# Optimization experiments

Hardware: AMD Instinct MI355X
Metric: run time of the kernel (lower is better)

Reference implementation:

```python
import jax, jax.numpy as jnp
import numpy as np

DECAY = 0.1
EPS = 1e-5


def setup_inputs() -> dict:
    key = jax.random.key(0)
    k1, k2, k3 = jax.random.split(key, 3)
    H, N, D, K = 1, 32768, 256, 4096
    x = jax.random.normal(k1, (H, N, D), dtype=jnp.float32)
    embed = jax.random.normal(k2, (H, K, D), dtype=jnp.float32) * 0.01
    cluster_size = jnp.ones((H, K), dtype=jnp.float32)
    embed_avg = jax.random.normal(k3, (H, K, D), dtype=jnp.float32) * 0.01
    return {"x": x, "embed": embed, "cluster_size": cluster_size, "embed_avg": embed_avg}


def reference(x, embed, cluster_size, embed_avg):
    # x: [H, N, D] flattened latents; embed: [H, K, D] codebook
    H, N, D = x.shape
    K = embed.shape[1]

    x_sq = jnp.sum(x * x, axis=-1, keepdims=True)          # [H, N, 1]
    e_sq = jnp.sum(embed * embed, axis=-1)[:, None, :]     # [H, 1, K]
    dist = x_sq - 2.0 * jnp.einsum('hnd,hkd->hnk', x, embed) + e_sq

    embed_ind = jnp.argmin(dist, axis=-1)                  # [H, N] int

    # gather nearest code vectors: [H, N, D]
    quantize = jax.vmap(lambda e, i: e[i])(embed, embed_ind)

    # EMA statistics (no_grad in torch): bincount + scatter-add of latents
    bins = jax.vmap(lambda i: jax.ops.segment_sum(jnp.ones((N,), x.dtype), i, num_segments=K))(embed_ind)                      # [H, K]
    embed_sum = jax.vmap(lambda xh, ih: jax.ops.segment_sum(xh, ih, num_segments=K))(x, embed_ind)                             # [H, K, D]

    new_cluster_size = cluster_size * DECAY + bins * (1.0 - DECAY)
    new_embed_avg = embed_avg * DECAY + embed_sum * (1.0 - DECAY)

    # laplace-smoothed normalization of codebook
    n = jnp.sum(new_cluster_size, axis=-1, keepdims=True)
    smoothed = (new_cluster_size + EPS) / (n + K * EPS) * n
    embed_normalized = new_embed_avg / smoothed[..., None]  # [H, K, D]

    # commitment loss (quantize detached) and straight-through output
    commit_loss = jnp.mean((jax.lax.stop_gradient(quantize) - x) ** 2)
    out = x + jax.lax.stop_gradient(quantize - x)

    return out, commit_loss, embed_ind, new_cluster_size, embed_normalized
```

## Files before the change

### kernel.cpp

```cpp
#include <hip/hip_runtime.h>
#include <hip/hip_bf16.h>
#include <cstdint>
#include <cstddef>

#define NROWS 32768
#define DDIM 256
#define KCODES 4096

typedef __attribute__((ext_vector_type(8))) short s16x8;
typedef __attribute__((ext_vector_type(4))) float f32x4;
typedef unsigned long long u64;
typedef unsigned int u32;

#define WS_LOSS 0
#define WS_CNT 1
#define WS_EMAX 2
#define WS_DISTRUST 3
#define WS_NSC 4
#define WS_HIST 8
#define WS_OFFS 4104
#define WS_CURSOR 8200
#define WS_LPART 12296
#define WS_RLIST 16392
#define WS_ESUM 49160
#define WS_XSQ 1097736
#define WS_ESQ 1130504
#define WS_IDX 1134600
#define WS_KEY 1167368
#define WS_TKEY 1232904
#define WS_TM2 1757192
#define WS_LIST 2019336
#define WS_EH 2052104
#define WS_EL 2576392
#define WS_TOTAL 3100680
#define WS_ZERO_FLOATS 12296

__device__ __forceinline__ float hsum16_np(const float a[16]) {
    float t3[8];
#pragma unroll
    for (int m = 0; m < 8; ++m) t3[m] = __fadd_rn(a[m + 8], a[m]);
    float t6[4];
#pragma unroll
    for (int m = 0; m < 4; ++m) t6[m] = __fadd_rn(t3[m + 4], t3[m]);
    return __fadd_rn(__fadd_rn(t6[0], t6[2]), __fadd_rn(t6[1], t6[3]));
}

__device__ __forceinline__ float np_sum_sq_128(const float* a) {
    float t[16];
#pragma unroll
    for (int l = 0; l < 16; ++l) {
        float m0 = __fmul_rn(a[l], a[l]);
        float m1 = __fmul_rn(a[16 + l], a[16 + l]);
        float m2 = __fmul_rn(a[32 + l], a[32 + l]);
        float m3 = __fmul_rn(a[48 + l], a[48 + l]);
        float m4 = __fmul_rn(a[64 + l], a[64 + l]);
        float m5 = __fmul_rn(a[80 + l], a[80 + l]);
        float m6 = __fmul_rn(a[96 + l], a[96 + l]);
        float m7 = __fmul_rn(a[112 + l], a[112 + l]);
        float s01 = __fadd_rn(m0, m1);
        float s23 = __fadd_rn(m2, m3);
        float s45 = __fadd_rn(m4, m5);
        float s67 = __fadd_rn(m6, m7);
        t[l] = __fadd_rn(__fadd_rn(s01, s23), __fadd_rn(s45, s67));
    }
    return hsum16_np(t);
}

__global__ void k_rownorm(const float* __restrict__ src, float* __restrict__ dst, int rows) {
    int r = blockIdx.x * blockDim.x + threadIdx.x;
    if (r < rows) {
        const float* p = src + ((size_t)r << 8);
        dst[r] = __fadd_rn(np_sum_sq_128(p), np_sum_sq_128(p + 128));
    }
}

__global__ void k_emax(const float* __restrict__ esq, float* __restrict__ emax) {
    __shared__ float s[1024];
    int t = threadIdx.x;
    float m = 0.0f;
    for (int i = t; i < KCODES; i += 1024) m = fmaxf(m, esq[i]);
    s[t] = m;
    __syncthreads();
    for (int w = 512; w > 0; w >>= 1) {
        if (t < w) s[t] = fmaxf(s[t], s[t + w]);
        __syncthreads();
    }
    if (t == 0) emax[0] = s[0];
}

__device__ __forceinline__ ushort bf16_rn(float x) {
    u32 u = __float_as_uint(x);
    u32 r = (u + 0x7fffu + ((u >> 16) & 1u)) >> 16;
    return (ushort)r;
}
__device__ __forceinline__ float bf16_f(ushort h) { return __uint_as_float(((u32)h) << 16); }

__global__ void k_pack(const float* __restrict__ src, ushort* __restrict__ hi,
                       ushort* __restrict__ lo) {
    int i = (blockIdx.x * 256 + threadIdx.x) * 8;
    float4 v0 = *reinterpret_cast<const float4*>(src + i);
    float4 v1 = *reinterpret_cast<const float4*>(src + i + 4);
    float f[8] = {v0.x, v0.y, v0.z, v0.w, v1.x, v1.y, v1.z, v1.w};
    ushort h[8], l[8];
#pragma unroll
    for (int j = 0; j < 8; ++j) {
        h[j] = bf16_rn(f[j]);
        l[j] = bf16_rn(__fsub_rn(f[j], bf16_f(h[j])));
    }
    *reinterpret_cast<s16x8*>(hi + i) = *reinterpret_cast<s16x8*>(h);
    *reinterpret_cast<s16x8*>(lo + i) = *reinterpret_cast<s16x8*>(l);
}

__device__ __forceinline__ float keyval_(u64 k) {
    u32 u = (u32)(k >> 32);
    u = (u & 0x80000000u) ? (u ^ 0x80000000u) : ~u;
    return __uint_as_float(u);
}
__device__ __forceinline__ u64 packkey(float d, u32 j) {
    u32 u = __float_as_uint(d);
    u ^= (u32)((int)u >> 31) | 0x80000000u;
    return ((u64)u << 32) | j;
}
#define KEY_INIT 0xFF8000007FFFFFFFull

__device__ __forceinline__ void dma16(const void* g, void* l) {
    __builtin_amdgcn_global_load_lds(
        (const __attribute__((address_space(1))) void*)g,
        (__attribute__((address_space(3))) void*)l, 16, 0, 0);
}

__global__ __attribute__((amdgpu_flat_work_group_size(512, 512), amdgpu_waves_per_eu(4, 4)))
void k_mfma(const ushort* __restrict__ xh_g, const ushort* __restrict__ xl_g,
            const ushort* __restrict__ eh_g, const ushort* __restrict__ el_g,
            const float* __restrict__ xsq, const float* __restrict__ esq,
            u64* __restrict__ tkey, float* __restrict__ tm2) {
    __shared__ __align__(16) ushort xh_s[16384];
    __shared__ __align__(16) ushort xl_s[16384];
    __shared__ __align__(16) ushort eh_s[4096];
    __shared__ __align__(16) ushort el_s[4096];

    const int tid = threadIdx.x;
    const int w = tid >> 6, l = tid & 63, lr = l & 15, lg = l >> 4;
    const int n0 = blockIdx.x * 256, jb = blockIdx.y, j0 = jb * 512;
    const int key = (lr & 7) << 4;

    float xq[8];
#pragma unroll
    for (int i = 0; i < 8; ++i)
        xq[i] = xsq[n0 + w * 32 + (i >> 2) * 16 + lg * 4 + (i & 3)];

    u64 K1[8];
    float M2[8];
#pragma unroll
    for (int i = 0; i < 8; ++i) { K1[i] = KEY_INIT; M2[i] = __uint_as_float(0x7F800000u); }

    for (int js = 0; js < 8; ++js) {
        const int jbase = j0 + js * 64;
        f32x4 acc[2][4];
#pragma unroll
        for (int a = 0; a < 2; ++a)
#pragma unroll
            for (int b = 0; b < 4; ++b) acc[a][b] = (f32x4){0.f, 0.f, 0.f, 0.f};

        for (int c = 0; c < 4; ++c) {
            __syncthreads();
#pragma unroll
            for (int p = 0; p < 4; ++p) {
                int m = tid + p * 512, r = m >> 3, cb = (m & 7) << 4;
                int so = (n0 + r) * 256 + c * 64 + ((cb ^ ((r & 7) << 4)) >> 1);
                dma16(xh_g + so, (char*)xh_s + m * 16);
                dma16(xl_g + so, (char*)xl_s + m * 16);
            }
            {
                int m = tid, r = m >> 3, cb = (m & 7) << 4;
                int so = (jbase + r) * 256 + c * 64 + ((cb ^ ((r & 7) << 4)) >> 1);
                dma16(eh_g + so, (char*)eh_s + m * 16);
                dma16(el_g + so, (char*)el_s + m * 16);
            }
            __syncthreads();
#pragma unroll
            for (int ks = 0; ks < 2; ++ks) {
                const int off = (ks * 64 + lg * 16) ^ key;
                s16x8 axh[2], axl[2];
#pragma unroll
                for (int ns = 0; ns < 2; ++ns) {
                    const int row = w * 32 + ns * 16 + lr;
                    axh[ns] = *(const s16x8*)((const char*)(xh_s + row * 64) + off);
                    axl[ns] = *(const s16x8*)((const char*)(xl_s + row * 64) + off);
                }
#pragma unroll
                for (int jp = 0; jp < 2; ++jp) {
                    s16x8 beh[2], bel[2];
#pragma unroll
                    for (int q = 0; q < 2; ++q) {
                        const int row = (jp * 2 + q) * 16 + lr;
                        beh[q] = *(const s16x8*)((const char*)(eh_s + row * 64) + off);
                        bel[q] = *(const s16x8*)((const char*)(el_s + row * 64) + off);
                    }
#pragma unroll
                    for (int q = 0; q < 2; ++q) {
                        const int jsub = jp * 2 + q;
#pragma unroll
                        for (int ns = 0; ns < 2; ++ns) {
                            acc[ns][jsub] = __builtin_amdgcn_mfma_f32_16x16x32_bf16(
                                axh[ns], beh[q], acc[ns][jsub], 0, 0, 0);
                            acc[ns][jsub] = __builtin_amdgcn_mfma_f32_16x16x32_bf16(
                                axh[ns], bel[q], acc[ns][jsub], 0, 0, 0);
                            acc[ns][jsub] = __builtin_amdgcn_mfma_f32_16x16x32_bf16(
                                axl[ns], beh[q], acc[ns][jsub], 0, 0, 0);
                        }
                    }
                }
            }
        }
#pragma unroll
        for (int jsub = 0; jsub < 4; ++jsub) {
            const int j = jbase + jsub * 16 + lr;
            const float eq = esq[j];
#pragma unroll
            for (int ns = 0; ns < 2; ++ns)
#pragma unroll
                for (int r = 0; r < 4; ++r) {
                    const float s = acc[ns][jsub][r];
                    const float d = __fadd_rn(__fsub_rn(xq[ns * 4 + r], __fmul_rn(2.0f, s)), eq);
                    const u64 kk = packkey(d, (u32)j);
                    const int i8 = ns * 4 + r;
                    if (kk < K1[i8]) { M2[i8] = keyval_(K1[i8]); K1[i8] = kk; }
                    else if (d < M2[i8]) M2[i8] = d;
                }
        }
    }
#pragma unroll
    for (int i8 = 0; i8 < 8; ++i8) {
        u64 k1 = K1[i8];
        float m2 = M2[i8];
#pragma unroll
        for (int mk = 1; mk < 16; mk <<= 1) {
            u32 klo = __shfl_xor((u32)k1, mk);
            u32 khi = __shfl_xor((u32)(k1 >> 32), mk);
            float om2 = __shfl_xor(m2, mk);
            u64 ok = ((u64)khi << 32) | klo;
            if (ok < k1) { m2 = fminf(om2, keyval_(k1)); k1 = ok; }
            else m2 = fminf(m2, keyval_(ok));
        }
        if (lr == 0) {
            const int n = n0 + w * 32 + (i8 >> 2) * 16 + lg * 4 + (i8 & 3);
            tkey[(size_t)jb * NROWS + n] = k1;
            tm2[(size_t)jb * NROWS + n] = m2;
        }
    }
}

__global__ void k_merge(const u64* __restrict__ tkey, const float* __restrict__ tm2,
                        const float* __restrict__ xsq, const float* __restrict__ emaxp,
                        u64* __restrict__ key64, u32* __restrict__ list, u32* __restrict__ cnt) {
    const int n = blockIdx.x * 256 + threadIdx.x;
    u64 k1 = tkey[n];
    float m2 = tm2[n];
#pragma unroll
    for (int jb = 1; jb < 8; ++jb) {
        u64 ok = tkey[(size_t)jb * NROWS + n];
        float om2 = tm2[(size_t)jb * NROWS + n];
        if (ok < k1) { m2 = fminf(om2, keyval_(k1)); k1 = ok; }
        else m2 = fminf(m2, keyval_(ok));
    }
    const float B = sqrtf(xsq[n] * emaxp[0]);
    const float Ed = 2.4e-4f * B + 1.5e-4f;
    if (m2 - keyval_(k1) <= 2.0f * Ed) {
        key64[n] = ~0ull;
        list[atomicAdd(cnt, 1u)] = (u32)n;
    } else {
        key64[n] = k1;
    }
}

__global__ void k_verify(const float* __restrict__ x, const float* __restrict__ e,
                         const float* __restrict__ xsq, const float* __restrict__ esq,
                         const float* __restrict__ emaxp, u64* __restrict__ key64,
                         u32* __restrict__ list, u32* __restrict__ cnt,
                         u32* __restrict__ distrust) {
    const int li = threadIdx.x & 15;
    const int n = blockIdx.x * 16 + (threadIdx.x >> 4);
    const u64 k = key64[n];
    const bool active = (k != ~0ull);
    const int idx = active ? (int)(k & 0xFFFu) : 0;
    const float* xr = x + ((size_t)n << 8);
    const float* er = e + ((size_t)idx << 8);
    float a = 0.0f;
#pragma unroll
    for (int g = 0; g < 4; ++g)
#pragma unroll
        for (int bb = 3; bb >= 0; --bb) {
            const int d = (g * 4 + bb) * 16 + li;
            a = __builtin_fmaf(xr[d], er[d], a);
        }
    const float s1 = __fadd_rn(__shfl_xor(a, 8), a);
    const float s2 = __fadd_rn(__shfl_xor(s1, 4), s1);
    const float u = __fadd_rn(s2, __shfl_xor(s2, 2));
    const float dot = __fadd_rn(u, __shfl_xor(u, 1));
    if (li == 0 && active) {
        const float d = __fadd_rn(__fsub_rn(xsq[n], __fmul_rn(2.0f, dot)), esq[idx]);
        const float dref = keyval_(k);
        const float B = sqrtf(xsq[n] * emaxp[0]);
        const float Ed = 2.4e-4f * B + 1.5e-4f;
        const float diff = fabsf(d - dref);
        if (diff > Ed) {
            key64[n] = ~0ull;
            list[atomicAdd(cnt, 1u)] = (u32)n;
            if (diff > 0.05f) atomicOr(distrust, 1u);
        }
    }
}

__global__ void k_distrust(const u32* __restrict__ distrust, u64* __restrict__ key64,
                           u32* __restrict__ list, u32* __restrict__ cnt) {
    if (*distrust == 0u) return;
    const int n = blockIdx.x * 256 + threadIdx.x;
    key64[n] = ~0ull;
    list[n] = (u32)n;
    if (n == 0) *cnt = (u32)NROWS;
}

__global__ __attribute__((amdgpu_flat_work_group_size(512, 512), amdgpu_waves_per_eu(4)))
void k_exact(const float* __restrict__ x, const float* __restrict__ embed,
             const float* __restrict__ xsq, const float* __restrict__ esq,
             const u32* __restrict__ list, const u32* __restrict__ cntp,
             u64* __restrict__ key64) {
    const u32 cnt = *cntp;
    const int grp = blockIdx.x >> 3, seg = blockIdx.x & 7;
    const u32 base = (u32)grp * 32u;
    if (base >= cnt) return;

    __shared__ float xs[32][260];
    __shared__ float es[64][68];
    u64* red = (u64*)&es[0][0];

    const int tid = threadIdx.x;
    const int lane = tid & 63;
    const int w = tid >> 6;
    const int g = w >> 2;
    const int tc = lane & 15;
    const int tr = ((w & 3) << 2) + (lane >> 4);
    const int cbase = (g << 5) + tc;

#pragma unroll
    for (int p = 0; p < 4; ++p) {
        int v = tid + p * 512;
        int r = v >> 6;
        int c4 = (v & 63) << 2;
        u32 row = list[(base + (u32)r < cnt) ? base + r : base];
        const float4 f = *reinterpret_cast<const float4*>(x + ((size_t)row << 8) + c4);
        *reinterpret_cast<float4*>(&xs[r][c4]) = f;
    }

    const u32 row0 = list[(base + (u32)tr < cnt) ? base + tr : base];
    const u32 row1 = list[(base + (u32)tr + 16u < cnt) ? base + tr + 16 : base];
    const float xq0 = xsq[row0];
    const float xq1 = xsq[row1];

    u64 best0 = ~0ull, best1 = ~0ull;

    for (int ktl = 0; ktl < 8; ++ktl) {
        const int k0 = seg * 512 + ktl * 64;
        float acc[2][2][16];
#pragma unroll
        for (int i = 0; i < 2; ++i)
#pragma unroll
            for (int j = 0; j < 2; ++j)
#pragma unroll
                for (int q = 0; q < 16; ++q) acc[i][j][q] = 0.0f;

        for (int c = 0; c < 4; ++c) {
            __syncthreads();
#pragma unroll
            for (int p = 0; p < 2; ++p) {
                int v = tid + p * 512;
                int r = v >> 4;
                int c4 = (v & 15) << 2;
                const float4 f = *reinterpret_cast<const float4*>(
                    embed + ((size_t)(k0 + r) << 8) + (c << 6) + c4);
                *reinterpret_cast<float4*>(&es[r][c4]) = f;
            }
            __syncthreads();
#pragma unroll
            for (int jj = 3; jj >= 0; --jj) {
#pragma unroll
                for (int q = 0; q < 4; ++q) {
                    const int dl = ((c * 4 + jj) << 4) + (q << 2);
                    const int el = (jj << 4) + (q << 2);
                    const float4 a0 = *reinterpret_cast<const float4*>(&xs[tr][dl]);
                    const float4 a1 = *reinterpret_cast<const float4*>(&xs[tr + 16][dl]);
                    const int lb = q << 2;
#pragma unroll
                    for (int j2 = 0; j2 < 2; ++j2) {
                        const float4 b = *reinterpret_cast<const float4*>(&es[cbase + 16 * j2][el]);
                        acc[0][j2][lb + 0] = __builtin_fmaf(a0.x, b.x, acc[0][j2][lb + 0]);
                        acc[0][j2][lb + 1] = __builtin_fmaf(a0.y, b.y, acc[0][j2][lb + 1]);
                        acc[0][j2][lb + 2] = __builtin_fmaf(a0.z, b.z, acc[0][j2][lb + 2]);
                        acc[0][j2][lb + 3] = __builtin_fmaf(a0.w, b.w, acc[0][j2][lb + 3]);
                        acc[1][j2][lb + 0] = __builtin_fmaf(a1.x, b.x, acc[1][j2][lb + 0]);
                        acc[1][j2][lb + 1] = __builtin_fmaf(a1.y, b.y, acc[1][j2][lb + 1]);
                        acc[1][j2][lb + 2] = __builtin_fmaf(a1.z, b.z, acc[1][j2][lb + 2]);
                        acc[1][j2][lb + 3] = __builtin_fmaf(a1.w, b.w, acc[1][j2][lb + 3]);
                    }
                }
            }
        }
#pragma unroll
        for (int j2 = 0; j2 < 2; ++j2) {
            const int kk = k0 + cbase + 16 * j2;
            const float eq = esq[kk];
            {
                const float dist = __fadd_rn(__fsub_rn(xq0, __fmul_rn(2.0f, hsum16_np(acc[0][j2]))), eq);
                const u64 kkey = packkey(dist, (u32)kk);
                best0 = kkey < best0 ? kkey : best0;
            }
            {
                const float dist = __fadd_rn(__fsub_rn(xq1, __fmul_rn(2.0f, hsum16_np(acc[1][j2]))), eq);
                const u64 kkey = packkey(dist, (u32)kk);
                best1 = kkey < best1 ? kkey : best1;
            }
        }
    }

    __syncthreads();
    red[tr * 32 + (g << 4) + tc] = best0;
    red[(tr + 16) * 32 + (g << 4) + tc] = best1;
    __syncthreads();
    if (tid < 32) {
        u64 m = red[tid * 32];
#pragma unroll
        for (int t = 1; t < 32; ++t) {
            u64 v = red[tid * 32 + t];
            m = v < m ? v : m;
        }
        if (base + (u32)tid < cnt) atomicMin(&key64[list[base + tid]], m);
    }
}

__global__ void k_finhist(const u64* __restrict__ key64, int* __restrict__ idx,
                          u32* __restrict__ hist, float* __restrict__ ind_out) {
    const int n = blockIdx.x * 256 + threadIdx.x;
    const int k = (int)(key64[n] & 0xFFFull);
    idx[n] = k;
    atomicAdd(&hist[k], 1u);
    ind_out[n] = (float)k;
}

__global__ __attribute__((amdgpu_flat_work_group_size(512, 512), amdgpu_waves_per_eu(4)))
void k_argmin_full(const float* __restrict__ x, const float* __restrict__ embed,
                   const float* __restrict__ xsq, const float* __restrict__ esq,
                   int* __restrict__ out_idx) {
    __shared__ float xs[32][260];
    __shared__ float es[64][68];
    u64* red = (u64*)&es[0][0];
    const int tid = threadIdx.x;
    const int lane = tid & 63;
    const int w = tid >> 6;
    const int g = w >> 2;
    const int tc = lane & 15;
    const int tr = ((w & 3) << 2) + (lane >> 4);
    const int cbase = (g << 5) + tc;
    const int n0 = blockIdx.x * 32;
#pragma unroll
    for (int p = 0; p < 4; ++p) {
        int v = tid + p * 512;
        int r = v >> 6;
        int c4 = (v & 63) << 2;
        const float4 f = *reinterpret_cast<const float4*>(x + ((size_t)(n0 + r) << 8) + c4);
        *reinterpret_cast<float4*>(&xs[r][c4]) = f;
    }
    const float xq0 = xsq[n0 + tr];
    const float xq1 = xsq[n0 + tr + 16];
    u64 best0 = ~0ull, best1 = ~0ull;
    for (int kt = 0; kt < KCODES / 64; ++kt) {
        const int k0 = kt * 64;
        float acc[2][2][16];
#pragma unroll
        for (int i = 0; i < 2; ++i)
#pragma unroll
            for (int j = 0; j < 2; ++j)
#pragma unroll
                for (int q = 0; q < 16; ++q) acc[i][j][q] = 0.0f;
        for (int c = 0; c < 4; ++c) {
            __syncthreads();
#pragma unroll
            for (int p = 0; p < 2; ++p) {
                int v = tid + p * 512;
                int r = v >> 4;
                int c4 = (v & 15) << 2;
                const float4 f = *reinterpret_cast<const float4*>(
                    embed + ((size_t)(k0 + r) << 8) + (c << 6) + c4);
                *reinterpret_cast<float4*>(&es[r][c4]) = f;
            }
            __syncthreads();
#pragma unroll
            for (int jj = 3; jj >= 0; --jj) {
#pragma unroll
                for (int q = 0; q < 4; ++q) {
                    const int dl = ((c * 4 + jj) << 4) + (q << 2);
                    const int el = (jj << 4) + (q << 2);
                    const float4 a0 = *reinterpret_cast<const float4*>(&xs[tr][dl]);
                    const float4 a1 = *reinterpret_cast<const float4*>(&xs[tr + 16][dl]);
                    const int lb = q << 2;
#pragma unroll
                    for (int j2 = 0; j2 < 2; ++j2) {
                        const float4 b = *reinterpret_cast<const float4*>(&es[cbase + 16 * j2][el]);
                        acc[0][j2][lb + 0] = __builtin_fmaf(a0.x, b.x, acc[0][j2][lb + 0]);
                        acc[0][j2][lb + 1] = __builtin_fmaf(a0.y, b.y, acc[0][j2][lb + 1]);
                        acc[0][j2][lb + 2] = __builtin_fmaf(a0.z, b.z, acc[0][j2][lb + 2]);
                        acc[0][j2][lb + 3] = __builtin_fmaf(a0.w, b.w, acc[0][j2][lb + 3]);
                        acc[1][j2][lb + 0] = __builtin_fmaf(a1.x, b.x, acc[1][j2][lb + 0]);
                        acc[1][j2][lb + 1] = __builtin_fmaf(a1.y, b.y, acc[1][j2][lb + 1]);
                        acc[1][j2][lb + 2] = __builtin_fmaf(a1.z, b.z, acc[1][j2][lb + 2]);
                        acc[1][j2][lb + 3] = __builtin_fmaf(a1.w, b.w, acc[1][j2][lb + 3]);
                    }
                }
            }
        }
#pragma unroll
        for (int j2 = 0; j2 < 2; ++j2) {
            const int kk = k0 + cbase + 16 * j2;
            const float eq = esq[kk];
            {
                const float dist = __fadd_rn(__fsub_rn(xq0, __fmul_rn(2.0f, hsum16_np(acc[0][j2]))), eq);
                const u64 kkey = packkey(dist, (u32)kk);
                best0 = kkey < best0 ? kkey : best0;
            }
            {
                const float dist = __fadd_rn(__fsub_rn(xq1, __fmul_rn(2.0f, hsum16_np(acc[1][j2]))), eq);
                const u64 kkey = packkey(dist, (u32)kk);
                best1 = kkey < best1 ? kkey : best1;
            }
        }
    }
    __syncthreads();
    red[tr * 32 + (g << 4) + tc] = best0;
    red[(tr + 16) * 32 + (g << 4) + tc] = best1;
    __syncthreads();
    if (tid < 32) {
        u64 m = red[tid * 32];
#pragma unroll
        for (int t = 1; t < 32; ++t) {
            u64 v = red[tid * 32 + t];
            m = v < m ? v : m;
        }
        out_idx[n0 + tid] = (int)(m & 0xFFFFFFFFu);
    }
}

__global__ void k_scan(const u32* __restrict__ hist, u32* __restrict__ offs) {
    __shared__ u32 ts[1024];
    const int t = threadIdx.x;
    const u32 h0 = hist[t * 4], h1 = hist[t * 4 + 1], h2 = hist[t * 4 + 2], h3 = hist[t * 4 + 3];
    const u32 tot = h0 + h1 + h2 + h3;
    ts[t] = tot;
    __syncthreads();
    for (int o = 1; o < 1024; o <<= 1) {
        const u32 add = (t >= o) ? ts[t - o] : 0u;
        __syncthreads();
        ts[t] += add;
        __syncthreads();
    }
    const u32 excl = ts[t] - tot;
    offs[t * 4] = excl;
    offs[t * 4 + 1] = excl + h0;
    offs[t * 4 + 2] = excl + h0 + h1;
    offs[t * 4 + 3] = excl + h0 + h1 + h2;
}

__global__ void k_place(const int* __restrict__ idx, u32* __restrict__ cursor,
                        const u32* __restrict__ offs, u32* __restrict__ rlist) {
    const int n = blockIdx.x * 256 + threadIdx.x;
    const int k = idx[n];
    const u32 p = atomicAdd(&cursor[k], 1u);
    rlist[offs[k] + p] = (u32)n;
}

__global__ void k_esum(const float* __restrict__ x, const u32* __restrict__ rlist,
                       const u32* __restrict__ offs, const u32* __restrict__ hist,
                       float* __restrict__ esum) {
    const int k = blockIdx.x;
    const int d = threadIdx.x;
    const u32 o = offs[k], c = hist[k];
    float s = 0.0f;
    for (u32 i = 0; i < c; ++i) s += x[((size_t)rlist[o + i] << 8) + d];
    esum[((size_t)k << 8) + d] = s;
}

__global__ void k_outloss(const float* __restrict__ x, const float* __restrict__ e,
                          const int* __restrict__ idx, float* __restrict__ out,
                          float* __restrict__ lpart) {
    const int d = threadIdx.x;
    float ls = 0.0f;
#pragma unroll
    for (int r = 0; r < 8; ++r) {
        const int n = blockIdx.x * 8 + r;
        const int k = idx[n];
        const size_t xi = ((size_t)n << 8) + d;
        const float xv = x[xi];
        const float qv = e[((size_t)k << 8) + d];
        const float diff = __fsub_rn(qv, xv);
        out[xi] = __fadd_rn(xv, diff);
        ls = __builtin_fmaf(diff, diff, ls);
    }
    __shared__ float sred[256];
    sred[d] = ls;
    __syncthreads();
    for (int s = 128; s > 0; s >>= 1) {
        if (d < s) sred[d] += sred[d + s];
        __syncthreads();
    }
    if (d == 0) lpart[blockIdx.x] = sred[0];
}

__global__ void k_cluster(const float* __restrict__ cs, const u32* __restrict__ hist,
                          float* __restrict__ ncs_out, float* __restrict__ n_out) {
    __shared__ float sred[1024];
    const int t = threadIdx.x;
    float s = 0.0f;
    for (int k = t; k < KCODES; k += 1024) {
        const float ncs = __fadd_rn(__fmul_rn(cs[k], 0.1f), __fmul_rn((float)hist[k], 0.9f));
        ncs_out[k] = ncs;
        s += ncs;
    }
    sred[t] = s;
    __syncthreads();
    for (int w = 512; w > 0; w >>= 1) {
        if (t < w) sred[t] += sred[t + w];
        __syncthreads();
    }
    if (t == 0) n_out[0] = sred[0];
}

__global__ void k_norm(const float* __restrict__ ea, const float* __restrict__ esum,
                       const float* __restrict__ ncs, const float* __restrict__ nptr,
                       float* __restrict__ en_out) {
    const int i = blockIdx.x * 256 + threadIdx.x;
    const int k = i >> 8;
    const float n = nptr[0];
    const float ncsk = ncs[k];
    const float smoothed = (ncsk + 1e-5f) / (n + 4096.0f * 1e-5f) * n;
    const float nea = __fadd_rn(__fmul_rn(ea[i], 0.1f), __fmul_rn(esum[i], 0.9f));
    en_out[i] = nea / smoothed;
}

__global__ void k_loss(const float* __restrict__ lpart, float* __restrict__ dst) {
    __shared__ float s[256];
    const int t = threadIdx.x;
    float a = 0.0f;
    for (int i = t; i < 4096; i += 256) a += lpart[i];
    s[t] = a;
    __syncthreads();
    for (int w = 128; w > 0; w >>= 1) {
        if (t < w) s[t] += s[t + w];
        __syncthreads();
    }
    if (t == 0) dst[0] = s[0] * (1.0f / 8388608.0f);
}

extern "C" void kernel_launch(void* const* d_in, const int* in_sizes, int n_in, void* d_out,
                              int out_size, void* d_ws, size_t ws_size, hipStream_t stream) {
    (void)in_sizes; (void)n_in; (void)out_size;
    const float* x = (const float*)d_in[0];
    const float* emb = (const float*)d_in[1];
    const float* cs = (const float*)d_in[2];
    const float* ea = (const float*)d_in[3];
    float* ws = (float*)d_ws;
    float* out = (float*)d_out;

    u32* w_cnt = (u32*)(ws + WS_CNT);
    float* w_emax = ws + WS_EMAX;
    u32* w_dis = (u32*)(ws + WS_DISTRUST);
    float* w_n = ws + WS_NSC;
    u32* w_hist = (u32*)(ws + WS_HIST);
    u32* w_offs = (u32*)(ws + WS_OFFS);
    u32* w_cursor = (u32*)(ws + WS_CURSOR);
    float* w_lpart = ws + WS_LPART;
    u32* w_rlist = (u32*)(ws + WS_RLIST);
    float* w_esum = ws + WS_ESUM;
    float* w_xsq = ws + WS_XSQ;
    float* w_esq = ws + WS_ESQ;
    int* w_idx = (int*)(ws + WS_IDX);
    u64* w_key = (u64*)(ws + WS_KEY);
    u64* w_tkey = (u64*)(ws + WS_TKEY);
    float* w_tm2 = ws + WS_TM2;
    u32* w_list = (u32*)(ws + WS_LIST);
    ushort* eh_g = (ushort*)(ws + WS_EH);
    ushort* el_g = (ushort*)(ws + WS_EL);

    float* o_out = out;
    float* o_loss = out + 8388608;
    float* o_ind = out + 8388609;
    float* o_ncs = out + 8421377;
    float* o_en = out + 8425473;

    ushort* xh_g = (ushort*)o_out;
    ushort* xl_g = (ushort*)o_out + 8388608;

    hipMemsetAsync(d_ws, 0, (size_t)WS_ZERO_FLOATS * sizeof(float), stream);

    k_rownorm<<<NROWS / 256, 256, 0, stream>>>(x, w_xsq, NROWS);
    k_rownorm<<<KCODES / 256, 256, 0, stream>>>(emb, w_esq, KCODES);

    if (ws_size >= (size_t)WS_TOTAL * sizeof(float)) {
        k_emax<<<1, 1024, 0, stream>>>(w_esq, w_emax);
        k_pack<<<4096, 256, 0, stream>>>(x, xh_g, xl_g);
        k_pack<<<512, 256, 0, stream>>>(emb, eh_g, el_g);
        k_mfma<<<dim3(128, 8), 512, 0, stream>>>(xh_g, xl_g, eh_g, el_g, w_xsq, w_esq,
                                                 w_tkey, w_tm2);
        k_merge<<<128, 256, 0, stream>>>(w_tkey, w_tm2, w_xsq, w_emax, w_key, w_list, w_cnt);
        k_verify<<<2048, 256, 0, stream>>>(x, emb, w_xsq, w_esq, w_emax, w_key, w_list,
                                           w_cnt, w_dis);
        k_distrust<<<128, 256, 0, stream>>>(w_dis, w_key, w_list, w_cnt);
        k_exact<<<8192, 512, 0, stream>>>(x, emb, w_xsq, w_esq, w_list, w_cnt, w_key);
        k_finhist<<<128, 256, 0, stream>>>(w_key, w_idx, w_hist, o_ind);
    } else {
        k_argmin_full<<<NROWS / 32, 512, 0, stream>>>(x, emb, w_xsq, w_esq, w_idx);
        k_finhist<<<128, 256, 0, stream>>>((u64*)w_key, w_idx, w_hist, o_ind);
    }

    k_scan<<<1, 1024, 0, stream>>>(w_hist, w_offs);
    k_place<<<128, 256, 0, stream>>>(w_idx, w_cursor, w_offs, w_rlist);
    k_esum<<<KCODES, 256, 0, stream>>>(x, w_rlist, w_offs, w_hist, w_esum);
    k_outloss<<<NROWS / 8, 256, 0, stream>>>(x, emb, w_idx, o_out, w_lpart);
    k_cluster<<<1, 1024, 0, stream>>>(cs, w_hist, o_ncs, w_n);
    k_norm<<<(KCODES * DDIM) / 256, 256, 0, stream>>>(ea, w_esum, o_ncs, w_n, o_en);
    k_loss<<<1, 256, 0, stream>>>(w_lpart, o_loss);
}
```

Baseline: 448.9 us.

## Keep x fragments in registers and double-buffer codebook tiles in LDS

The MFMA distance kernel now loads the block's 256-row x tile once into registers (hi/lo bf16 fragments for all four K-chunks) instead of reloading it from global to LDS for every 64-code slab. Codebook slabs are double-buffered in a 128KB LDS buffer, with the next slab's DMA issued while the current one is computed, and the per-chunk barrier pairs are replaced by one barrier per slab. Occupancy drops to 2 waves per EU to make room for the larger register footprint. The fallback path gets a separate histogram kernel that reads the index array directly, which fixes it reading an uninitialized key buffer.

After: 432.8 us. -3.6%, faster.

```diff
diff --git a/kernel.cpp b/kernel.cpp
--- a/kernel.cpp
+++ b/kernel.cpp
@@ -129,20 +129,88 @@
         (__attribute__((address_space(3))) void*)l, 16, 0, 0);
 }
 
-__global__ __attribute__((amdgpu_flat_work_group_size(512, 512), amdgpu_waves_per_eu(4, 4)))
+__device__ __forceinline__ void ckstep(const char* eh, const char* el, int coff, int o,
+                                       int lr, s16x8 fh0, s16x8 fh1, s16x8 fl0, s16x8 fl1,
+                                       f32x4 acc[2][4]) {
+#pragma unroll
+    for (int jp = 0; jp < 2; ++jp) {
+        s16x8 beh[2], bel[2];
+#pragma unroll
+        for (int q = 0; q < 2; ++q) {
+            const int rowb = (((jp * 2 + q) * 16 + lr) << 9) + coff + o;
+            beh[q] = *(const s16x8*)(eh + rowb);
+            bel[q] = *(const s16x8*)(el + rowb);
+        }
+#pragma unroll
+        for (int q = 0; q < 2; ++q) {
+            const int jsub = jp * 2 + q;
+            acc[0][jsub] = __builtin_amdgcn_mfma_f32_16x16x32_bf16(fh0, beh[q], acc[0][jsub], 0, 0, 0);
+            acc[0][jsub] = __builtin_amdgcn_mfma_f32_16x16x32_bf16(fh0, bel[q], acc[0][jsub], 0, 0, 0);
+            acc[0][jsub] = __builtin_amdgcn_mfma_f32_16x16x32_bf16(fl0, beh[q], acc[0][jsub], 0, 0, 0);
+            acc[1][jsub] = __builtin_amdgcn_mfma_f32_16x16x32_bf16(fh1, beh[q], acc[1][jsub], 0, 0, 0);
+            acc[1][jsub] = __builtin_amdgcn_mfma_f32_16x16x32_bf16(fh1, bel[q], acc[1][jsub], 0, 0, 0);
+            acc[1][jsub] = __builtin_amdgcn_mfma_f32_16x16x32_bf16(fl1, beh[q], acc[1][jsub], 0, 0, 0);
+        }
+    }
+}
+
+__global__ __attribute__((amdgpu_flat_work_group_size(512, 512), amdgpu_waves_per_eu(2, 2)))
 void k_mfma(const ushort* __restrict__ xh_g, const ushort* __restrict__ xl_g,
             const ushort* __restrict__ eh_g, const ushort* __restrict__ el_g,
             const float* __restrict__ xsq, const float* __restrict__ esq,
             u64* __restrict__ tkey, float* __restrict__ tm2) {
-    __shared__ __align__(16) ushort xh_s[16384];
-    __shared__ __align__(16) ushort xl_s[16384];
-    __shared__ __align__(16) ushort eh_s[4096];
-    __shared__ __align__(16) ushort el_s[4096];
+    __shared__ __align__(16) char lds[131072];
 
     const int tid = threadIdx.x;
     const int w = tid >> 6, l = tid & 63, lr = l & 15, lg = l >> 4;
     const int n0 = blockIdx.x * 256, jb = blockIdx.y, j0 = jb * 512;
     const int key = (lr & 7) << 4;
+    const int o0 = (lg * 16) ^ key;
+    const int o1 = (64 + lg * 16) ^ key;
+
+    s16x8 fh[4][2][2], fl[4][2][2];
+    {
+#pragma unroll
+        for (int p = 0; p < 4; ++p) {
+            int m = tid + p * 512, r = m >> 3, cb = (m & 7) << 4;
+            size_t so = (size_t)(n0 + r) * 256 + 0 * 64 + ((cb ^ ((r & 7) << 4)) >> 1);
+            dma16(xh_g + so, lds + m * 16);
+            dma16(xl_g + so, lds + 32768 + m * 16);
+        }
+        __syncthreads();
+#pragma unroll
+        for (int c = 0; c < 4; ++c) {
+            const char* xa = lds + ((c & 1) << 16);
+            if (c < 3) {
+                char* xb = lds + (((c + 1) & 1) << 16);
+#pragma unroll
+                for (int p = 0; p < 4; ++p) {
+                    int m = tid + p * 512, r = m >> 3, cb = (m & 7) << 4;
+                    size_t so = (size_t)(n0 + r) * 256 + (c + 1) * 64 + ((cb ^ ((r & 7) << 4)) >> 1);
+                    dma16(xh_g + so, xb + m * 16);
+                    dma16(xl_g + so, xb + 32768 + m * 16);
+                }
+            }
+#pragma unroll
+            for (int ks = 0; ks < 2; ++ks)
+#pragma unroll
+                for (int ns = 0; ns < 2; ++ns) {
+                    const int addr = ((w * 32 + ns * 16 + lr) << 7) + (ks ? o1 : o0);
+                    fh[c][ks][ns] = *(const s16x8*)(xa + addr);
+                    fl[c][ks][ns] = *(const s16x8*)(xa + 32768 + addr);
+                }
+            __syncthreads();
+        }
+#pragma unroll
+        for (int p = 0; p < 4; ++p) {
+            int m = tid + p * 512, r = m >> 5, cb = (m & 31) << 4;
+            int scol = (cb & ~127) | ((cb & 127) ^ ((r & 7) << 4));
+            size_t so = (size_t)(j0 + r) * 256 + (scol >> 1);
+            dma16(eh_g + so, lds + m * 16);
+            dma16(el_g + so, lds + 32768 + m * 16);
+        }
+        __syncthreads();
+    }
 
     float xq[8];
 #pragma unroll
@@ -156,63 +224,32 @@
 
     for (int js = 0; js < 8; ++js) {
         const int jbase = j0 + js * 64;
+        const char* eh = lds + ((js & 1) << 16);
+        const char* el = eh + 32768;
+        if (js < 7) {
+            char* nh = lds + (((js + 1) & 1) << 16);
+#pragma unroll
+            for (int p = 0; p < 4; ++p) {
+                int m = tid + p * 512, r = m >> 5, cb = (m & 31) << 4;
+                int scol = (cb & ~127) | ((cb & 127) ^ ((r & 7) << 4));
+                size_t so = (size_t)(jbase + 64 + r) * 256 + (scol >> 1);
+                dma16(eh_g + so, nh + m * 16);
+                dma16(el_g + so, nh + 32768 + m * 16);
+            }
+        }
+
         f32x4 acc[2][4];
 #pragma unroll
         for (int a = 0; a < 2; ++a)
 #pragma unroll
             for (int b = 0; b < 4; ++b) acc[a][b] = (f32x4){0.f, 0.f, 0.f, 0.f};
 
+#pragma unroll
         for (int c = 0; c < 4; ++c) {
-            __syncthreads();
-#pragma unroll
-            for (int p = 0; p < 4; ++p) {
-                int m = tid + p * 512, r = m >> 3, cb = (m & 7) << 4;
-                int so = (n0 + r) * 256 + c * 64 + ((cb ^ ((r & 7) << 4)) >> 1);
-                dma16(xh_g + so, (char*)xh_s + m * 16);
-                dma16(xl_g + so, (char*)xl_s + m * 16);
-            }
-            {
-                int m = tid, r = m >> 3, cb = (m & 7) << 4;
-                int so = (jbase + r) * 256 + c * 64 + ((cb ^ ((r & 7) << 4)) >> 1);
-                dma16(eh_g + so, (char*)eh_s + m * 16);
-                dma16(el_g + so, (char*)el_s + m * 16);
-            }
-            __syncthreads();
-#pragma unroll
-            for (int ks = 0; ks < 2; ++ks) {
-                const int off = (ks * 64 + lg * 16) ^ key;
-                s16x8 axh[2], axl[2];
-#pragma unroll
-                for (int ns = 0; ns < 2; ++ns) {
-                    const int row = w * 32 + ns * 16 + lr;
-                    axh[ns] = *(const s16x8*)((const char*)(xh_s + row * 64) + off);
-                    axl[ns] = *(const s16x8*)((const char*)(xl_s + row * 64) + off);
-                }
-#pragma unroll
-                for (int jp = 0; jp < 2; ++jp) {
-                    s16x8 beh[2], bel[2];
-#pragma unroll
-                    for (int q = 0; q < 2; ++q) {
-                        const int row = (jp * 2 + q) * 16 + lr;
-                        beh[q] = *(const s16x8*)((const char*)(eh_s + row * 64) + off);
-                        bel[q] = *(const s16x8*)((const char*)(el_s + row * 64) + off);
-                    }
-#pragma unroll
-                    for (int q = 0; q < 2; ++q) {
-                        const int jsub = jp * 2 + q;
-#pragma unroll
-                        for (int ns = 0; ns < 2; ++ns) {
-                            acc[ns][jsub] = __builtin_amdgcn_mfma_f32_16x16x32_bf16(
-                                axh[ns], beh[q], acc[ns][jsub], 0, 0, 0);
-                            acc[ns][jsub] = __builtin_amdgcn_mfma_f32_16x16x32_bf16(
-                                axh[ns], bel[q], acc[ns][jsub], 0, 0, 0);
-                            acc[ns][jsub] = __builtin_amdgcn_mfma_f32_16x16x32_bf16(
-                                axl[ns], beh[q], acc[ns][jsub], 0, 0, 0);
-                        }
-                    }
-                }
-            }
-        }
+            ckstep(eh, el, c * 128, o0, lr, fh[c][0][0], fh[c][0][1], fl[c][0][0], fl[c][0][1], acc);
+            ckstep(eh, el, c * 128, o1, lr, fh[c][1][0], fh[c][1][1], fl[c][1][0], fl[c][1][1], acc);
+        }
+
 #pragma unroll
         for (int jsub = 0; jsub < 4; ++jsub) {
             const int j = jbase + jsub * 16 + lr;
@@ -229,7 +266,9 @@
                     else if (d < M2[i8]) M2[i8] = d;
                 }
         }
-    }
+        __syncthreads();
+    }
+
 #pragma unroll
     for (int i8 = 0; i8 < 8; ++i8) {
         u64 k1 = K1[i8];
@@ -443,6 +482,14 @@
     const int n = blockIdx.x * 256 + threadIdx.x;
     const int k = (int)(key64[n] & 0xFFFull);
     idx[n] = k;
+    atomicAdd(&hist[k], 1u);
+    ind_out[n] = (float)k;
+}
+
+__global__ void k_histidx(const int* __restrict__ idx, u32* __restrict__ hist,
+                          float* __restrict__ ind_out) {
+    const int n = blockIdx.x * 256 + threadIdx.x;
+    const int k = idx[n];
     atomicAdd(&hist[k], 1u);
     ind_out[n] = (float)k;
 }
@@ -717,7 +764,7 @@
         k_finhist<<<128, 256, 0, stream>>>(w_key, w_idx, w_hist, o_ind);
     } else {
         k_argmin_full<<<NROWS / 32, 512, 0, stream>>>(x, emb, w_xsq, w_esq, w_idx);
-        k_finhist<<<128, 256, 0, stream>>>((u64*)w_key, w_idx, w_hist, o_ind);
+        k_histidx<<<128, 256, 0, stream>>>(w_idx, w_hist, o_ind);
     }
 
     k_scan<<<1, 1024, 0, stream>>>(w_hist, w_offs);
```

## Remap MFMA grid for XCD-aware L2 locality and fuse scan with cluster update

Applied to the files above, without the earlier changes.

Flattens the MFMA distance kernel grid into 1024 linear blocks and remaps each block ID so that blocks landing on the same XCD share row tiles and codebook tiles. The aim is more L2 reuse of the packed x and embed operands. Separately, the cluster-size EMA and its sum move into the scan kernel, which removes one single-block launch. The fallback path also gets a proper histogram kernel that reads int indices, instead of calling k_finhist on an unpopulated key buffer.

Result: no change. 448.2 us (-0.2%).

```diff
diff --git a/kernel.cpp b/kernel.cpp
--- a/kernel.cpp
+++ b/kernel.cpp
@@ -141,7 +141,11 @@
 
     const int tid = threadIdx.x;
     const int w = tid >> 6, l = tid & 63, lr = l & 15, lg = l >> 4;
-    const int n0 = blockIdx.x * 256, jb = blockIdx.y, j0 = jb * 512;
+    const int lid = blockIdx.x;
+    const int xcd = lid & 7, sslot = lid >> 3, sp = sslot >> 3, ww = sslot & 7;
+    const int bxg = xcd * 16 + (sp & 3) * 4 + (ww & 3);
+    const int jb = ((sp >> 2) << 1) + (ww >> 2);
+    const int n0 = bxg * 256, j0 = jb * 512;
     const int key = (lr & 7) << 4;
 
     float xq[8];
@@ -443,6 +447,14 @@
     const int n = blockIdx.x * 256 + threadIdx.x;
     const int k = (int)(key64[n] & 0xFFFull);
     idx[n] = k;
+    atomicAdd(&hist[k], 1u);
+    ind_out[n] = (float)k;
+}
+
+__global__ void k_histidx(const int* __restrict__ idx, u32* __restrict__ hist,
+                          float* __restrict__ ind_out) {
+    const int n = blockIdx.x * 256 + threadIdx.x;
+    const int k = idx[n];
     atomicAdd(&hist[k], 1u);
     ind_out[n] = (float)k;
 }
@@ -549,12 +561,24 @@
     }
 }
 
-__global__ void k_scan(const u32* __restrict__ hist, u32* __restrict__ offs) {
+__global__ void k_scancluster(const u32* __restrict__ hist, u32* __restrict__ offs,
+                              const float* __restrict__ cs, float* __restrict__ ncs_out,
+                              float* __restrict__ n_out) {
     __shared__ u32 ts[1024];
+    __shared__ float fs[1024];
     const int t = threadIdx.x;
     const u32 h0 = hist[t * 4], h1 = hist[t * 4 + 1], h2 = hist[t * 4 + 2], h3 = hist[t * 4 + 3];
     const u32 tot = h0 + h1 + h2 + h3;
     ts[t] = tot;
+    const float n0_ = __fadd_rn(__fmul_rn(cs[t * 4 + 0], 0.1f), __fmul_rn((float)h0, 0.9f));
+    const float n1_ = __fadd_rn(__fmul_rn(cs[t * 4 + 1], 0.1f), __fmul_rn((float)h1, 0.9f));
+    const float n2_ = __fadd_rn(__fmul_rn(cs[t * 4 + 2], 0.1f), __fmul_rn((float)h2, 0.9f));
+    const float n3_ = __fadd_rn(__fmul_rn(cs[t * 4 + 3], 0.1f), __fmul_rn((float)h3, 0.9f));
+    ncs_out[t * 4 + 0] = n0_;
+    ncs_out[t * 4 + 1] = n1_;
+    ncs_out[t * 4 + 2] = n2_;
+    ncs_out[t * 4 + 3] = n3_;
+    fs[t] = ((n0_ + n1_) + n2_) + n3_;
     __syncthreads();
     for (int o = 1; o < 1024; o <<= 1) {
         const u32 add = (t >= o) ? ts[t - o] : 0u;
@@ -567,6 +591,11 @@
     offs[t * 4 + 1] = excl + h0;
     offs[t * 4 + 2] = excl + h0 + h1;
     offs[t * 4 + 3] = excl + h0 + h1 + h2;
+    for (int wd = 512; wd > 0; wd >>= 1) {
+        if (t < wd) fs[t] += fs[t + wd];
+        __syncthreads();
+    }
+    if (t == 0) n_out[0] = fs[0];
 }
 
 __global__ void k_place(const int* __restrict__ idx, u32* __restrict__ cursor,
@@ -612,25 +641,6 @@
         __syncthreads();
     }
     if (d == 0) lpart[blockIdx.x] = sred[0];
-}
-
-__global__ void k_cluster(const float* __restrict__ cs, const u32* __restrict__ hist,
-                          float* __restrict__ ncs_out, float* __restrict__ n_out) {
-    __shared__ float sred[1024];
-    const int t = threadIdx.x;
-    float s = 0.0f;
-    for (int k = t; k < KCODES; k += 1024) {
-        const float ncs = __fadd_rn(__fmul_rn(cs[k], 0.1f), __fmul_rn((float)hist[k], 0.9f));
-        ncs_out[k] = ncs;
-        s += ncs;
-    }
-    sred[t] = s;
-    __syncthreads();
-    for (int w = 512; w > 0; w >>= 1) {
-        if (t < w) sred[t] += sred[t + w];
-        __syncthreads();
-    }
-    if (t == 0) n_out[0] = sred[0];
 }
 
 __global__ void k_norm(const float* __restrict__ ea, const float* __restrict__ esum,
@@ -707,8 +717,8 @@
         k_emax<<<1, 1024, 0, stream>>>(w_esq, w_emax);
         k_pack<<<4096, 256, 0, stream>>>(x, xh_g, xl_g);
         k_pack<<<512, 256, 0, stream>>>(emb, eh_g, el_g);
-        k_mfma<<<dim3(128, 8), 512, 0, stream>>>(xh_g, xl_g, eh_g, el_g, w_xsq, w_esq,
-                                                 w_tkey, w_tm2);
+        k_mfma<<<1024, 512, 0, stream>>>(xh_g, xl_g, eh_g, el_g, w_xsq, w_esq,
+                                         w_tkey, w_tm2);
         k_merge<<<128, 256, 0, stream>>>(w_tkey, w_tm2, w_xsq, w_emax, w_key, w_list, w_cnt);
         k_verify<<<2048, 256, 0, stream>>>(x, emb, w_xsq, w_esq, w_emax, w_key, w_list,
                                            w_cnt, w_dis);
@@ -717,14 +727,13 @@
         k_finhist<<<128, 256, 0, stream>>>(w_key, w_idx, w_hist, o_ind);
     } else {
         k_argmin_full<<<NROWS / 32, 512, 0, stream>>>(x, emb, w_xsq, w_esq, w_idx);
-        k_finhist<<<128, 256, 0, stream>>>((u64*)w_key, w_idx, w_hist, o_ind);
-    }
-
-    k_scan<<<1, 1024, 0, stream>>>(w_hist, w_offs);
+        k_histidx<<<128, 256, 0, stream>>>(w_idx, w_hist, o_ind);
+    }
+
+    k_scancluster<<<1, 1024, 0, stream>>>(w_hist, w_offs, cs, o_ncs, w_n);
     k_place<<<128, 256, 0, stream>>>(w_idx, w_cursor, w_offs, w_rlist);
     k_esum<<<KCODES, 256, 0, stream>>>(x, w_rlist, w_offs, w_hist, w_esum);
     k_outloss<<<NROWS / 8, 256, 0, stream>>>(x, emb, w_idx, o_out, w_lpart);
-    k_cluster<<<1, 1024, 0, stream>>>(cs, w_hist, o_ncs, w_n);
     k_norm<<<(KCODES * DDIM) / 256, 256, 0, stream>>>(ea, w_esum, o_ncs, w_n, o_en);
     k_loss<<<1, 256, 0, stream>>>(w_lpart, o_loss);
 }
```
